# Kernel tuning notes

Measured on AMD Instinct MI355X. Metric: run time of the kernel, lower is better.

The kernel has to match this reference:

```python
import jax, jax.numpy as jnp
import numpy as np

B, C, T = 8, 256, 8192
CALC, H = 256, 4
D = CALC // H  # head dim = 64
EPS = 1e-5


def setup_inputs() -> dict:
    key = jax.random.key(0)
    ks = jax.random.split(key, 5)
    return {
        "x": jax.random.normal(ks[0], (B, C, T), dtype=jnp.float32),
        "W_prenet": jax.random.normal(ks[1], (3 * CALC, C), dtype=jnp.float32) * 0.05,
        "W_proj": jax.random.normal(ks[2], (C, CALC), dtype=jnp.float32) * 0.05,
        "b_proj": jax.random.normal(ks[3], (C,), dtype=jnp.float32) * 0.05,
        "scale": jax.random.normal(ks[4], (1,), dtype=jnp.float32),
        "gamma": jnp.ones((C,), dtype=jnp.float32),
        "beta": jnp.zeros((C,), dtype=jnp.float32),
    }


def reference(x, W_prenet, W_proj, b_proj, scale, gamma, beta):
    residual = x
    # 1x1 conv prenet: [B, 3*CALC, T]
    h = jnp.einsum('oc,bct->bot', W_prenet, x)
    # split heads: channels grouped as H blocks of 3*D, then chunk into q/k/v of D each
    h = h.reshape(B, H, 3 * D, T)
    q = h[:, :, :D, :]            # [B,H,D,T]
    k = h[:, :, D:2 * D, :]
    v = h[:, :, 2 * D:, :]
    # softmax over time on keys (with the module's +1e-5 shift)
    k = jax.nn.softmax(k + EPS, axis=3)
    # keys @ values^T : [B,H,Dk,Dv]
    kv = jnp.einsum('bhdt,bhet->bhde', k, v)
    # kv^T @ queries  : [B,H,Dv,T]
    ctx = jnp.einsum('bhde,bhdt->bhet', kv, q)
    ctx = ctx.reshape(B, CALC, T)
    # 1x1 conv projection + bias
    out = jnp.einsum('oc,bct->bot', W_proj, ctx) + b_proj[None, :, None]
    out = scale * out  # learnable scalar gate
    # dropout is identity in eval mode
    out = out + residual
    # LayerNorm over channel axis with per-channel affine
    mean = jnp.mean(out, axis=1, keepdims=True)
    var = jnp.var(out, axis=1, keepdims=True)
    out = (out - mean) * jax.lax.rsqrt(var + EPS)
    out = out * gamma[None, :, None] + beta[None, :, None]
    return out
```

## Files before the change

kernel.cpp:

```cpp
#include <hip/hip_runtime.h>
#include <hip/hip_bf16.h>
#include <math.h>

#define BB 8
#define CC 256
#define TT 8192
#define EPSF 1e-5f

typedef short v8s __attribute__((ext_vector_type(8)));
typedef float v4f __attribute__((ext_vector_type(4)));

#define MFMA(a, b, c) __builtin_amdgcn_mfma_f32_16x16x32_bf16((a), (b), (c), 0, 0, 0)


#define OFF_WKV 0
#define OFF_WPJ 65536
#define OFF_UPART 98304
#define OFF_ZPART 4292608
#define OFF_KV 4358144
#define OFF_PT 4489216
#define OFF_MBF 4751360

__device__ __forceinline__ unsigned short f2bf(float f) {
  __hip_bfloat16 h = __float2bfloat16(f);
  return __builtin_bit_cast(unsigned short, h);
}
__device__ __forceinline__ float bf2f(unsigned short u) {
  return __bfloat162float(__builtin_bit_cast(__hip_bfloat16, u));
}

__global__ void k0_pack(const float* __restrict__ Wpre,
                        const float* __restrict__ Wproj,
                        float* __restrict__ ws) {
  const int r = blockIdx.x;
  const int c = threadIdx.x;
  if (r < 512) {
    const int h = r >> 7, type = (r >> 6) & 1, d = r & 63;
    const int src = h * 192 + 64 + type * 64 + d;
    ((unsigned short*)(ws + OFF_WKV))[r * 256 + c] = f2bf(Wpre[(size_t)src * 256 + c]);
  } else {
    const int rr = r - 512;
    ((unsigned short*)(ws + OFF_WPJ))[rr * 256 + c] = f2bf(Wproj[(size_t)rr * 256 + c]);
  }
}

__global__ __launch_bounds__(512, 2) void k1_kv(const float* __restrict__ x,
                                                float* __restrict__ ws) {
  __shared__ unsigned short lds[20480];

  const int tid = threadIdx.x;
  const int w = tid >> 6, lane = tid & 63, q = lane >> 4, cl = lane & 15;
  const int h = w >> 1, type = w & 1;
  const int bi = blockIdx.x;
  const int b = bi >> 5, chunk = bi & 31;
  const int t0 = chunk * 256;
  const float* xb = x + (size_t)b * (CC * TT);
  const unsigned short* wkv =
      (const unsigned short*)(ws + OFF_WKV) + (size_t)((h * 2 + type) * 64) * 256;
  unsigned short* ekb = &lds[h * 5120];
  unsigned short* vbb = &lds[h * 5120 + 2560];

  v4f Uacc[2][4];
#pragma unroll
  for (int i = 0; i < 2; ++i)
#pragma unroll
    for (int j = 0; j < 4; ++j) Uacc[i][j] = (v4f){0.f, 0.f, 0.f, 0.f};
  float zacc[4][4];
#pragma unroll
  for (int i = 0; i < 4; ++i)
#pragma unroll
    for (int j = 0; j < 4; ++j) zacc[i][j] = 0.f;

  for (int sub = 0; sub < 4; ++sub) {
    const int ts = t0 + sub * 64;
    {
      const int c = tid & 255, th = tid >> 8;
      const float* xp = xb + (size_t)c * TT + ts + th * 32;
#pragma unroll
      for (int j = 0; j < 8; ++j) {
        const float4 v4 = reinterpret_cast<const float4*>(xp)[j];
        const int tb = th * 32 + j * 4;
        lds[(tb + 0) * 264 + c] = f2bf(v4.x);
        lds[(tb + 1) * 264 + c] = f2bf(v4.y);
        lds[(tb + 2) * 264 + c] = f2bf(v4.z);
        lds[(tb + 3) * 264 + c] = f2bf(v4.w);
      }
    }
    __syncthreads();

    v4f acc[4][4];
#pragma unroll
    for (int i = 0; i < 4; ++i)
#pragma unroll
      for (int j = 0; j < 4; ++j) acc[i][j] = (v4f){0.f, 0.f, 0.f, 0.f};
#pragma unroll
    for (int ks = 0; ks < 8; ++ks) {
      v8s af[4], bfu[4];
#pragma unroll
      for (int rt = 0; rt < 4; ++rt)
        af[rt] = *(const v8s*)(wkv + (size_t)(rt * 16 + cl) * 256 + ks * 32 + q * 8);
#pragma unroll
      for (int ct = 0; ct < 4; ++ct)
        bfu[ct] = *(const v8s*)&lds[(ct * 16 + cl) * 264 + ks * 32 + q * 8];
#pragma unroll
      for (int rt = 0; rt < 4; ++rt)
#pragma unroll
        for (int ct = 0; ct < 4; ++ct)
          acc[rt][ct] = MFMA(af[rt], bfu[ct], acc[rt][ct]);
    }
    __syncthreads();

#pragma unroll
    for (int hp = 0; hp < 2; ++hp) {
      if (type == 0) {
#pragma unroll
        for (int rt = 0; rt < 4; ++rt)
#pragma unroll
          for (int cc = 0; cc < 2; ++cc) {
            const int ct = hp * 2 + cc;
#pragma unroll
            for (int reg = 0; reg < 4; ++reg) {
              const float e = __expf(acc[rt][ct][reg]);
              zacc[rt][reg] += e;
              ekb[(rt * 16 + q * 4 + reg) * 40 + cc * 16 + cl] = f2bf(e);
            }
          }
      } else {
#pragma unroll
        for (int rt = 0; rt < 4; ++rt)
#pragma unroll
          for (int cc = 0; cc < 2; ++cc) {
            const int ct = hp * 2 + cc;
#pragma unroll
            for (int reg = 0; reg < 4; ++reg)
              vbb[(rt * 16 + q * 4 + reg) * 40 + cc * 16 + cl] =
                  f2bf(acc[rt][ct][reg]);
          }
      }
      __syncthreads();
      {
        const int du0 = type * 32;
        v8s afu[2], bfu[4];
#pragma unroll
        for (int ur = 0; ur < 2; ++ur)
          afu[ur] = *(const v8s*)&ekb[(du0 + ur * 16 + cl) * 40 + q * 8];
#pragma unroll
        for (int uc = 0; uc < 4; ++uc)
          bfu[uc] = *(const v8s*)&vbb[(uc * 16 + cl) * 40 + q * 8];
#pragma unroll
        for (int ur = 0; ur < 2; ++ur)
#pragma unroll
          for (int uc = 0; uc < 4; ++uc)
            Uacc[ur][uc] = MFMA(afu[ur], bfu[uc], Uacc[ur][uc]);
      }
      __syncthreads();
    }
  }

  if (type == 0) {
#pragma unroll
    for (int m = 1; m < 16; m <<= 1)
#pragma unroll
      for (int rt = 0; rt < 4; ++rt)
#pragma unroll
        for (int reg = 0; reg < 4; ++reg)
          zacc[rt][reg] += __shfl_xor(zacc[rt][reg], m, 64);
    if (cl == 0) {
      for (int rt = 0; rt < 4; ++rt)
        for (int reg = 0; reg < 4; ++reg)
          ws[OFF_ZPART + (size_t)bi * 256 + h * 64 + rt * 16 + q * 4 + reg] =
              zacc[rt][reg];
    }
  }
  float* Up = ws + OFF_UPART + (size_t)bi * 16384 + h * 4096;
#pragma unroll
  for (int ur = 0; ur < 2; ++ur)
#pragma unroll
    for (int uc = 0; uc < 4; ++uc)
#pragma unroll
      for (int reg = 0; reg < 4; ++reg)
        Up[(type * 32 + ur * 16 + q * 4 + reg) * 64 + uc * 16 + cl] =
            Uacc[ur][uc][reg];
}

__global__ void k2_reduce_kv(float* __restrict__ ws) {
  const int bi = blockIdx.x;
  const int bh = bi >> 4, j = bi & 15;
  const int b = bh >> 2, h = bh & 3;
  const int tid = threadIdx.x;

  __shared__ float zinv[64];
  if (tid < 64) {
    float z = 0.f;
    for (int cb = 0; cb < 32; ++cb)
      z += ws[OFF_ZPART + (size_t)(b * 32 + cb) * 256 + h * 64 + tid];
    zinv[tid] = 1.0f / z;
  }
  __syncthreads();

  const int idx = j * 256 + tid;
  const int d = idx >> 6;
  float s = 0.f;
  for (int cb = 0; cb < 32; ++cb)
    s += ws[OFF_UPART + (size_t)(b * 32 + cb) * 16384 + h * 4096 + idx];
  ws[OFF_KV + (size_t)(b * 4 + h) * 4096 + idx] = s * zinv[d];
}

__global__ void k3a_P(const float* __restrict__ Wpre, float* __restrict__ ws) {
  const int bi = blockIdx.x;
  const int b = bi >> 8, he = bi & 255;
  const int h = he >> 6, e = he & 63;
  const int c = threadIdx.x;
  const float* kvp = ws + OFF_KV + (size_t)(b * 4 + h) * 4096;
  float acc = 0.f;
#pragma unroll 8
  for (int d = 0; d < 64; ++d)
    acc += kvp[d * 64 + e] * Wpre[(size_t)(h * 192 + d) * 256 + c];
  ((unsigned short*)(ws + OFF_PT))[(size_t)b * 65536 + (size_t)c * 256 + he] =
      f2bf(acc);
}

__global__ __launch_bounds__(256, 2) void k3b_M(const float* __restrict__ scale,
                                                float* __restrict__ ws) {
  const int bi = blockIdx.x, b = bi >> 2, cg = bi & 3;
  const int tid = threadIdx.x, w = tid >> 6, lane = tid & 63, q = lane >> 4,
            cl = lane & 15;
  const unsigned short* wpj = (const unsigned short*)(ws + OFF_WPJ);
  const unsigned short* pt =
      (const unsigned short*)(ws + OFF_PT) + (size_t)b * 65536;
  v4f acc[4][4];
#pragma unroll
  for (int i = 0; i < 4; ++i)
#pragma unroll
    for (int j = 0; j < 4; ++j) acc[i][j] = (v4f){0.f, 0.f, 0.f, 0.f};
#pragma unroll
  for (int ks = 0; ks < 8; ++ks) {
    v8s af[4], bfu[4];
#pragma unroll
    for (int rt = 0; rt < 4; ++rt)
      af[rt] = *(const v8s*)(wpj + (size_t)(w * 64 + rt * 16 + cl) * 256 +
                             ks * 32 + q * 8);
#pragma unroll
    for (int ct = 0; ct < 4; ++ct)
      bfu[ct] = *(const v8s*)(pt + (size_t)(cg * 64 + ct * 16 + cl) * 256 +
                              ks * 32 + q * 8);
#pragma unroll
    for (int rt = 0; rt < 4; ++rt)
#pragma unroll
      for (int ct = 0; ct < 4; ++ct)
        acc[rt][ct] = MFMA(af[rt], bfu[ct], acc[rt][ct]);
  }
  const float s = scale[0];
  unsigned short* mbf = (unsigned short*)(ws + OFF_MBF);
#pragma unroll
  for (int rt = 0; rt < 4; ++rt)
#pragma unroll
    for (int ct = 0; ct < 4; ++ct)
#pragma unroll
      for (int reg = 0; reg < 4; ++reg) {
        const int o = w * 64 + rt * 16 + q * 4 + reg;
        const int c = cg * 64 + ct * 16 + cl;
        mbf[((size_t)b * 256 + o) * 256 + c] = f2bf(s * acc[rt][ct][reg]);
      }
}

__global__ __launch_bounds__(256, 2) void k4_proj_ln(
    const float* __restrict__ x, const float* __restrict__ bproj,
    const float* __restrict__ scale, const float* __restrict__ gamma,
    const float* __restrict__ beta, const float* __restrict__ ws,
    float* __restrict__ out) {
  __shared__ unsigned short xs[64 * 264];
  __shared__ float red1[256], red2[256], muA[64], rsA[64];
  const int bi = blockIdx.x, b = bi >> 7, tc = bi & 127;
  const int tg0 = tc * 64;
  const int tid = threadIdx.x, w = tid >> 6, lane = tid & 63, q = lane >> 4,
            cl = lane & 15;
  const float* xb = x + (size_t)b * (CC * TT);

  {
    const int c = tid;
    const float* xp = xb + (size_t)c * TT + tg0;
#pragma unroll
    for (int j = 0; j < 16; ++j) {
      const float4 v4 = reinterpret_cast<const float4*>(xp)[j];
      const int tb = j * 4;
      xs[(tb + 0) * 264 + c] = f2bf(v4.x);
      xs[(tb + 1) * 264 + c] = f2bf(v4.y);
      xs[(tb + 2) * 264 + c] = f2bf(v4.z);
      xs[(tb + 3) * 264 + c] = f2bf(v4.w);
    }
  }
  __syncthreads();

  const unsigned short* mbf =
      (const unsigned short*)(ws + OFF_MBF) + (size_t)b * 65536;
  v4f acc[4][4];
#pragma unroll
  for (int i = 0; i < 4; ++i)
#pragma unroll
    for (int j = 0; j < 4; ++j) acc[i][j] = (v4f){0.f, 0.f, 0.f, 0.f};
#pragma unroll
  for (int ks = 0; ks < 8; ++ks) {
    v8s af[4], bfu[4];
#pragma unroll
    for (int rt = 0; rt < 4; ++rt)
      af[rt] = *(const v8s*)(mbf + (size_t)(w * 64 + rt * 16 + cl) * 256 +
                             ks * 32 + q * 8);
#pragma unroll
    for (int ct = 0; ct < 4; ++ct)
      bfu[ct] = *(const v8s*)&xs[(ct * 16 + cl) * 264 + ks * 32 + q * 8];
#pragma unroll
    for (int rt = 0; rt < 4; ++rt)
#pragma unroll
      for (int ct = 0; ct < 4; ++ct)
        acc[rt][ct] = MFMA(af[rt], bfu[ct], acc[rt][ct]);
  }

  const float s = scale[0];
#pragma unroll
  for (int rt = 0; rt < 4; ++rt)
#pragma unroll
    for (int reg = 0; reg < 4; ++reg) {
      const int o = w * 64 + rt * 16 + q * 4 + reg;
      const float sb = s * bproj[o];
#pragma unroll
      for (int ct = 0; ct < 4; ++ct) {
        const int tl = ct * 16 + cl;
        acc[rt][ct][reg] += sb + bf2f(xs[tl * 264 + o]);
      }
    }

#pragma unroll
  for (int ct = 0; ct < 4; ++ct) {
    float s1 = 0.f, s2 = 0.f;
#pragma unroll
    for (int rt = 0; rt < 4; ++rt)
#pragma unroll
      for (int reg = 0; reg < 4; ++reg) {
        const float v = acc[rt][ct][reg];
        s1 += v;
        s2 += v * v;
      }
    s1 += __shfl_xor(s1, 16, 64);
    s1 += __shfl_xor(s1, 32, 64);
    s2 += __shfl_xor(s2, 16, 64);
    s2 += __shfl_xor(s2, 32, 64);
    if (q == 0) {
      red1[w * 64 + ct * 16 + cl] = s1;
      red2[w * 64 + ct * 16 + cl] = s2;
    }
  }
  __syncthreads();
  if (tid < 64) {
    const float s1 = red1[tid] + red1[64 + tid] + red1[128 + tid] + red1[192 + tid];
    const float s2 = red2[tid] + red2[64 + tid] + red2[128 + tid] + red2[192 + tid];
    const float mu = s1 * (1.f / 256.f);
    const float var = s2 * (1.f / 256.f) - mu * mu;
    muA[tid] = mu;
    rsA[tid] = rsqrtf(var + EPSF);
  }
  __syncthreads();

  float* ob = out + (size_t)b * (CC * TT) + tg0;
#pragma unroll
  for (int rt = 0; rt < 4; ++rt)
#pragma unroll
    for (int reg = 0; reg < 4; ++reg) {
      const int o = w * 64 + rt * 16 + q * 4 + reg;
      const float g = gamma[o], bt = beta[o];
#pragma unroll
      for (int ct = 0; ct < 4; ++ct) {
        const int tl = ct * 16 + cl;
        ob[(size_t)o * TT + tl] = (acc[rt][ct][reg] - muA[tl]) * rsA[tl] * g + bt;
      }
    }
}

extern "C" void kernel_launch(void* const* d_in, const int* in_sizes, int n_in,
                              void* d_out, int out_size, void* d_ws,
                              size_t ws_size, hipStream_t stream) {
  (void)in_sizes; (void)n_in; (void)out_size; (void)ws_size;
  const float* x = (const float*)d_in[0];
  const float* Wpre = (const float*)d_in[1];
  const float* Wproj = (const float*)d_in[2];
  const float* bproj = (const float*)d_in[3];
  const float* scale = (const float*)d_in[4];
  const float* gamma = (const float*)d_in[5];
  const float* beta = (const float*)d_in[6];
  float* out = (float*)d_out;
  float* ws = (float*)d_ws;

  hipLaunchKernelGGL(k0_pack, dim3(768), dim3(256), 0, stream, Wpre, Wproj, ws);
  hipLaunchKernelGGL(k1_kv, dim3(256), dim3(512), 0, stream, x, ws);
  hipLaunchKernelGGL(k2_reduce_kv, dim3(512), dim3(256), 0, stream, ws);
  hipLaunchKernelGGL(k3a_P, dim3(BB * 256), dim3(256), 0, stream, Wpre, ws);
  hipLaunchKernelGGL(k3b_M, dim3(32), dim3(256), 0, stream, scale, ws);
  hipLaunchKernelGGL(k4_proj_ln, dim3(BB * 128), dim3(256), 0, stream, x, bproj,
                     scale, gamma, beta, ws, out);
}
```

Baseline: 222.5 us.

## Split kernels into more blocks and pack bf16 pairs in LDS staging

Doubles the grid of the KV kernel (128-step time chunks, 64 partials per batch) and the projection/LayerNorm kernel (32-column tiles), and splits the M GEMM across 4x more blocks. The aim is more parallelism and occupancy on a GPU with many CUs. It also replaces 16-bit LDS stores with paired 32-bit stores of two channels, cutting LDS store instructions. The cost is double the partial-sum traffic and reduction work in k2, a larger workspace, and less MFMA operand reuse per block.

```diff
diff --git a/kernel.cpp b/kernel.cpp
--- a/kernel.cpp
+++ b/kernel.cpp
@@ -16,10 +16,10 @@
 #define OFF_WKV 0
 #define OFF_WPJ 65536
 #define OFF_UPART 98304
-#define OFF_ZPART 4292608
-#define OFF_KV 4358144
-#define OFF_PT 4489216
-#define OFF_MBF 4751360
+#define OFF_ZPART 8486912
+#define OFF_KV 8617984
+#define OFF_PT 8749056
+#define OFF_MBF 9011200
 
 __device__ __forceinline__ unsigned short f2bf(float f) {
   __hip_bfloat16 h = __float2bfloat16(f);
@@ -27,6 +27,9 @@
 }
 __device__ __forceinline__ float bf2f(unsigned short u) {
   return __bfloat162float(__builtin_bit_cast(__hip_bfloat16, u));
+}
+__device__ __forceinline__ unsigned int pack2(float lo, float hi) {
+  return (unsigned int)f2bf(lo) | ((unsigned int)f2bf(hi) << 16);
 }
 
 __global__ void k0_pack(const float* __restrict__ Wpre,
@@ -44,7 +47,7 @@
   }
 }
 
-__global__ __launch_bounds__(512, 2) void k1_kv(const float* __restrict__ x,
+__global__ __launch_bounds__(512, 4) void k1_kv(const float* __restrict__ x,
                                                 float* __restrict__ ws) {
   __shared__ unsigned short lds[20480];
 
@@ -52,8 +55,8 @@
   const int w = tid >> 6, lane = tid & 63, q = lane >> 4, cl = lane & 15;
   const int h = w >> 1, type = w & 1;
   const int bi = blockIdx.x;
-  const int b = bi >> 5, chunk = bi & 31;
-  const int t0 = chunk * 256;
+  const int b = bi >> 6, chunk = bi & 63;
+  const int t0 = chunk * 128;
   const float* xb = x + (size_t)b * (CC * TT);
   const unsigned short* wkv =
       (const unsigned short*)(ws + OFF_WKV) + (size_t)((h * 2 + type) * 64) * 256;
@@ -71,19 +74,25 @@
 #pragma unroll
     for (int j = 0; j < 4; ++j) zacc[i][j] = 0.f;
 
-  for (int sub = 0; sub < 4; ++sub) {
+  const int c0 = (tid & 127) * 2;
+  const int th = tid >> 7;
+  unsigned int* l32 = (unsigned int*)lds;
+
+  for (int sub = 0; sub < 2; ++sub) {
     const int ts = t0 + sub * 64;
     {
-      const int c = tid & 255, th = tid >> 8;
-      const float* xp = xb + (size_t)c * TT + ts + th * 32;
-#pragma unroll
-      for (int j = 0; j < 8; ++j) {
-        const float4 v4 = reinterpret_cast<const float4*>(xp)[j];
-        const int tb = th * 32 + j * 4;
-        lds[(tb + 0) * 264 + c] = f2bf(v4.x);
-        lds[(tb + 1) * 264 + c] = f2bf(v4.y);
-        lds[(tb + 2) * 264 + c] = f2bf(v4.z);
-        lds[(tb + 3) * 264 + c] = f2bf(v4.w);
+      const float* xpA = xb + (size_t)c0 * TT + ts + th * 16;
+      const float* xpB = xpA + TT;
+      const int cw = c0 >> 1;
+#pragma unroll
+      for (int k = 0; k < 4; ++k) {
+        const float4 va = reinterpret_cast<const float4*>(xpA)[k];
+        const float4 vb = reinterpret_cast<const float4*>(xpB)[k];
+        const int tb = th * 16 + k * 4;
+        l32[(tb + 0) * 132 + cw] = pack2(va.x, vb.x);
+        l32[(tb + 1) * 132 + cw] = pack2(va.y, vb.y);
+        l32[(tb + 2) * 132 + cw] = pack2(va.z, vb.z);
+        l32[(tb + 3) * 132 + cw] = pack2(va.w, vb.w);
       }
     }
     __syncthreads();
@@ -192,8 +201,8 @@
   __shared__ float zinv[64];
   if (tid < 64) {
     float z = 0.f;
-    for (int cb = 0; cb < 32; ++cb)
-      z += ws[OFF_ZPART + (size_t)(b * 32 + cb) * 256 + h * 64 + tid];
+    for (int cb = 0; cb < 64; ++cb)
+      z += ws[OFF_ZPART + (size_t)(b * 64 + cb) * 256 + h * 64 + tid];
     zinv[tid] = 1.0f / z;
   }
   __syncthreads();
@@ -201,8 +210,8 @@
   const int idx = j * 256 + tid;
   const int d = idx >> 6;
   float s = 0.f;
-  for (int cb = 0; cb < 32; ++cb)
-    s += ws[OFF_UPART + (size_t)(b * 32 + cb) * 16384 + h * 4096 + idx];
+  for (int cb = 0; cb < 64; ++cb)
+    s += ws[OFF_UPART + (size_t)(b * 64 + cb) * 16384 + h * 4096 + idx];
   ws[OFF_KV + (size_t)(b * 4 + h) * 4096 + idx] = s * zinv[d];
 }
 
@@ -222,97 +231,94 @@
 
 __global__ __launch_bounds__(256, 2) void k3b_M(const float* __restrict__ scale,
                                                 float* __restrict__ ws) {
-  const int bi = blockIdx.x, b = bi >> 2, cg = bi & 3;
+  const int bi = blockIdx.x;
+  const int b = bi >> 4, cg = (bi >> 2) & 3, rg = bi & 3;
   const int tid = threadIdx.x, w = tid >> 6, lane = tid & 63, q = lane >> 4,
             cl = lane & 15;
   const unsigned short* wpj = (const unsigned short*)(ws + OFF_WPJ);
   const unsigned short* pt =
       (const unsigned short*)(ws + OFF_PT) + (size_t)b * 65536;
-  v4f acc[4][4];
-#pragma unroll
-  for (int i = 0; i < 4; ++i)
-#pragma unroll
-    for (int j = 0; j < 4; ++j) acc[i][j] = (v4f){0.f, 0.f, 0.f, 0.f};
+  v4f acc[4];
+#pragma unroll
+  for (int j = 0; j < 4; ++j) acc[j] = (v4f){0.f, 0.f, 0.f, 0.f};
 #pragma unroll
   for (int ks = 0; ks < 8; ++ks) {
-    v8s af[4], bfu[4];
-#pragma unroll
-    for (int rt = 0; rt < 4; ++rt)
-      af[rt] = *(const v8s*)(wpj + (size_t)(w * 64 + rt * 16 + cl) * 256 +
-                             ks * 32 + q * 8);
+    const v8s af = *(const v8s*)(wpj + (size_t)(rg * 64 + w * 16 + cl) * 256 +
+                                 ks * 32 + q * 8);
+    v8s bfu[4];
 #pragma unroll
     for (int ct = 0; ct < 4; ++ct)
       bfu[ct] = *(const v8s*)(pt + (size_t)(cg * 64 + ct * 16 + cl) * 256 +
                               ks * 32 + q * 8);
 #pragma unroll
-    for (int rt = 0; rt < 4; ++rt)
-#pragma unroll
-      for (int ct = 0; ct < 4; ++ct)
-        acc[rt][ct] = MFMA(af[rt], bfu[ct], acc[rt][ct]);
+    for (int ct = 0; ct < 4; ++ct) acc[ct] = MFMA(af, bfu[ct], acc[ct]);
   }
   const float s = scale[0];
   unsigned short* mbf = (unsigned short*)(ws + OFF_MBF);
 #pragma unroll
-  for (int rt = 0; rt < 4; ++rt)
-#pragma unroll
-    for (int ct = 0; ct < 4; ++ct)
-#pragma unroll
-      for (int reg = 0; reg < 4; ++reg) {
-        const int o = w * 64 + rt * 16 + q * 4 + reg;
-        const int c = cg * 64 + ct * 16 + cl;
-        mbf[((size_t)b * 256 + o) * 256 + c] = f2bf(s * acc[rt][ct][reg]);
-      }
-}
-
-__global__ __launch_bounds__(256, 2) void k4_proj_ln(
+  for (int ct = 0; ct < 4; ++ct)
+#pragma unroll
+    for (int reg = 0; reg < 4; ++reg) {
+      const int o = rg * 64 + w * 16 + q * 4 + reg;
+      const int c = cg * 64 + ct * 16 + cl;
+      mbf[((size_t)b * 256 + o) * 256 + c] = f2bf(s * acc[ct][reg]);
+    }
+}
+
+__global__ __launch_bounds__(256, 4) void k4_proj_ln(
     const float* __restrict__ x, const float* __restrict__ bproj,
     const float* __restrict__ scale, const float* __restrict__ gamma,
     const float* __restrict__ beta, const float* __restrict__ ws,
     float* __restrict__ out) {
-  __shared__ unsigned short xs[64 * 264];
-  __shared__ float red1[256], red2[256], muA[64], rsA[64];
-  const int bi = blockIdx.x, b = bi >> 7, tc = bi & 127;
-  const int tg0 = tc * 64;
+  __shared__ unsigned short xs[32 * 264];
+  __shared__ float red1[128], red2[128], muA[32], rsA[32];
+  const int bi = blockIdx.x, b = bi >> 8, tc = bi & 255;
+  const int tg0 = tc * 32;
   const int tid = threadIdx.x, w = tid >> 6, lane = tid & 63, q = lane >> 4,
             cl = lane & 15;
   const float* xb = x + (size_t)b * (CC * TT);
 
   {
-    const int c = tid;
-    const float* xp = xb + (size_t)c * TT + tg0;
-#pragma unroll
-    for (int j = 0; j < 16; ++j) {
-      const float4 v4 = reinterpret_cast<const float4*>(xp)[j];
-      const int tb = j * 4;
-      xs[(tb + 0) * 264 + c] = f2bf(v4.x);
-      xs[(tb + 1) * 264 + c] = f2bf(v4.y);
-      xs[(tb + 2) * 264 + c] = f2bf(v4.z);
-      xs[(tb + 3) * 264 + c] = f2bf(v4.w);
+    const int c0 = (tid & 127) * 2;
+    const int th = tid >> 7;
+    const float* xpA = xb + (size_t)c0 * TT + tg0 + th * 16;
+    const float* xpB = xpA + TT;
+    unsigned int* x32 = (unsigned int*)xs;
+    const int cw = c0 >> 1;
+#pragma unroll
+    for (int k = 0; k < 4; ++k) {
+      const float4 va = reinterpret_cast<const float4*>(xpA)[k];
+      const float4 vb = reinterpret_cast<const float4*>(xpB)[k];
+      const int tb = th * 16 + k * 4;
+      x32[(tb + 0) * 132 + cw] = pack2(va.x, vb.x);
+      x32[(tb + 1) * 132 + cw] = pack2(va.y, vb.y);
+      x32[(tb + 2) * 132 + cw] = pack2(va.z, vb.z);
+      x32[(tb + 3) * 132 + cw] = pack2(va.w, vb.w);
     }
   }
   __syncthreads();
 
   const unsigned short* mbf =
       (const unsigned short*)(ws + OFF_MBF) + (size_t)b * 65536;
-  v4f acc[4][4];
+  v4f acc[4][2];
 #pragma unroll
   for (int i = 0; i < 4; ++i)
 #pragma unroll
-    for (int j = 0; j < 4; ++j) acc[i][j] = (v4f){0.f, 0.f, 0.f, 0.f};
+    for (int j = 0; j < 2; ++j) acc[i][j] = (v4f){0.f, 0.f, 0.f, 0.f};
 #pragma unroll
   for (int ks = 0; ks < 8; ++ks) {
-    v8s af[4], bfu[4];
+    v8s af[4], bfu[2];
 #pragma unroll
     for (int rt = 0; rt < 4; ++rt)
       af[rt] = *(const v8s*)(mbf + (size_t)(w * 64 + rt * 16 + cl) * 256 +
                              ks * 32 + q * 8);
 #pragma unroll
-    for (int ct = 0; ct < 4; ++ct)
+    for (int ct = 0; ct < 2; ++ct)
       bfu[ct] = *(const v8s*)&xs[(ct * 16 + cl) * 264 + ks * 32 + q * 8];
 #pragma unroll
     for (int rt = 0; rt < 4; ++rt)
 #pragma unroll
-      for (int ct = 0; ct < 4; ++ct)
+      for (int ct = 0; ct < 2; ++ct)
         acc[rt][ct] = MFMA(af[rt], bfu[ct], acc[rt][ct]);
   }
 
@@ -324,14 +330,14 @@
       const int o = w * 64 + rt * 16 + q * 4 + reg;
       const float sb = s * bproj[o];
 #pragma unroll
-      for (int ct = 0; ct < 4; ++ct) {
+      for (int ct = 0; ct < 2; ++ct) {
         const int tl = ct * 16 + cl;
         acc[rt][ct][reg] += sb + bf2f(xs[tl * 264 + o]);
       }
     }
 
 #pragma unroll
-  for (int ct = 0; ct < 4; ++ct) {
+  for (int ct = 0; ct < 2; ++ct) {
     float s1 = 0.f, s2 = 0.f;
 #pragma unroll
     for (int rt = 0; rt < 4; ++rt)
@@ -346,14 +352,14 @@
     s2 += __shfl_xor(s2, 16, 64);
     s2 += __shfl_xor(s2, 32, 64);
     if (q == 0) {
-      red1[w * 64 + ct * 16 + cl] = s1;
-      red2[w * 64 + ct * 16 + cl] = s2;
+      red1[w * 32 + ct * 16 + cl] = s1;
+      red2[w * 32 + ct * 16 + cl] = s2;
     }
   }
   __syncthreads();
-  if (tid < 64) {
-    const float s1 = red1[tid] + red1[64 + tid] + red1[128 + tid] + red1[192 + tid];
-    const float s2 = red2[tid] + red2[64 + tid] + red2[128 + tid] + red2[192 + tid];
+  if (tid < 32) {
+    const float s1 = red1[tid] + red1[32 + tid] + red1[64 + tid] + red1[96 + tid];
+    const float s2 = red2[tid] + red2[32 + tid] + red2[64 + tid] + red2[96 + tid];
     const float mu = s1 * (1.f / 256.f);
     const float var = s2 * (1.f / 256.f) - mu * mu;
     muA[tid] = mu;
@@ -369,7 +375,7 @@
       const int o = w * 64 + rt * 16 + q * 4 + reg;
       const float g = gamma[o], bt = beta[o];
 #pragma unroll
-      for (int ct = 0; ct < 4; ++ct) {
+      for (int ct = 0; ct < 2; ++ct) {
         const int tl = ct * 16 + cl;
         ob[(size_t)o * TT + tl] = (acc[rt][ct][reg] - muA[tl]) * rsA[tl] * g + bt;
       }
@@ -391,10 +397,10 @@
   float* ws = (float*)d_ws;
 
   hipLaunchKernelGGL(k0_pack, dim3(768), dim3(256), 0, stream, Wpre, Wproj, ws);
-  hipLaunchKernelGGL(k1_kv, dim3(256), dim3(512), 0, stream, x, ws);
+  hipLaunchKernelGGL(k1_kv, dim3(512), dim3(512), 0, stream, x, ws);
   hipLaunchKernelGGL(k2_reduce_kv, dim3(512), dim3(256), 0, stream, ws);
   hipLaunchKernelGGL(k3a_P, dim3(BB * 256), dim3(256), 0, stream, Wpre, ws);
-  hipLaunchKernelGGL(k3b_M, dim3(32), dim3(256), 0, stream, scale, ws);
-  hipLaunchKernelGGL(k4_proj_ln, dim3(BB * 128), dim3(256), 0, stream, x, bproj,
-                     scale, gamma, beta, ws, out);
-}
+  hipLaunchKernelGGL(k3b_M, dim3(128), dim3(256), 0, stream, scale, ws);
+  hipLaunchKernelGGL(k4_proj_ln, dim3(BB * 128 * 2), dim3(256), 0, stream, x,
+                     bproj, scale, gamma, beta, ws, out);
+}
```

Result: slower. 287.8 us (+29.4%).

## Split k1_kv work by head pair across more blocks and prefetch next x tile

Applied to the files above, without the earlier changes.

The KV-accumulation kernel now launches twice as many blocks, each handling two heads instead of four, with each warp computing a 16-row slice of both K and V projections instead of a whole K or V head. The x tile for the next sub-step is loaded into registers while the U MFMA runs, then written to LDS as packed bf16 pairs, replacing the per-iteration blocking load. The aim is more parallelism across CUs, less per-warp register pressure, and overlap of global loads with compute. In exchange, x is read twice (once per head pair) and the reduce kernel's indexing changes to match.

```diff
diff --git a/kernel.cpp b/kernel.cpp
--- a/kernel.cpp
+++ b/kernel.cpp
@@ -27,6 +27,9 @@
 }
 __device__ __forceinline__ float bf2f(unsigned short u) {
   return __bfloat162float(__builtin_bit_cast(__hip_bfloat16, u));
+}
+__device__ __forceinline__ unsigned int pack2(float lo, float hi) {
+  return (unsigned int)f2bf(lo) | ((unsigned int)f2bf(hi) << 16);
 }
 
 __global__ void k0_pack(const float* __restrict__ Wpre,
@@ -44,156 +47,166 @@
   }
 }
 
-__global__ __launch_bounds__(512, 2) void k1_kv(const float* __restrict__ x,
-                                                float* __restrict__ ws) {
-  __shared__ unsigned short lds[20480];
+__global__ __launch_bounds__(512) void k1_kv(const float* __restrict__ x,
+                                             float* __restrict__ ws) {
+  __shared__ unsigned short lds[35328];
 
   const int tid = threadIdx.x;
   const int w = tid >> 6, lane = tid & 63, q = lane >> 4, cl = lane & 15;
-  const int h = w >> 1, type = w & 1;
+  const int lh = w >> 2, dq = w & 3;
   const int bi = blockIdx.x;
-  const int b = bi >> 5, chunk = bi & 31;
+  const int b = bi >> 6, rem = bi & 63, chunk = rem >> 1, hp = rem & 1;
+  const int h = hp * 2 + lh;
   const int t0 = chunk * 256;
   const float* xb = x + (size_t)b * (CC * TT);
-  const unsigned short* wkv =
-      (const unsigned short*)(ws + OFF_WKV) + (size_t)((h * 2 + type) * 64) * 256;
-  unsigned short* ekb = &lds[h * 5120];
-  unsigned short* vbb = &lds[h * 5120 + 2560];
-
-  v4f Uacc[2][4];
-#pragma unroll
-  for (int i = 0; i < 2; ++i)
-#pragma unroll
-    for (int j = 0; j < 4; ++j) Uacc[i][j] = (v4f){0.f, 0.f, 0.f, 0.f};
-  float zacc[4][4];
-#pragma unroll
-  for (int i = 0; i < 4; ++i)
-#pragma unroll
-    for (int j = 0; j < 4; ++j) zacc[i][j] = 0.f;
+  const unsigned short* wk =
+      (const unsigned short*)(ws + OFF_WKV) + (size_t)((h * 2 + 0) * 64) * 256;
+  const unsigned short* wv =
+      (const unsigned short*)(ws + OFF_WKV) + (size_t)((h * 2 + 1) * 64) * 256;
+  unsigned short* eb = &lds[16896 + lh * 9216];
+  unsigned short* vb = &lds[16896 + lh * 9216 + 4608];
+
+  v4f Uacc[4];
+#pragma unroll
+  for (int j = 0; j < 4; ++j) Uacc[j] = (v4f){0.f, 0.f, 0.f, 0.f};
+  float zacc[4] = {0.f, 0.f, 0.f, 0.f};
+
+  const int c0 = (tid & 127) * 2;
+  const int th = tid >> 7;
+  const int cw = tid & 127;
+  unsigned int* l32 = (unsigned int*)lds;
+
+  {
+    const float* xpA = xb + (size_t)c0 * TT + t0 + th * 16;
+    const float* xpB = xpA + TT;
+#pragma unroll
+    for (int k = 0; k < 4; ++k) {
+      const float4 va = reinterpret_cast<const float4*>(xpA)[k];
+      const float4 vb4 = reinterpret_cast<const float4*>(xpB)[k];
+      const int tb = th * 16 + k * 4;
+      l32[(tb + 0) * 132 + cw] = pack2(va.x, vb4.x);
+      l32[(tb + 1) * 132 + cw] = pack2(va.y, vb4.y);
+      l32[(tb + 2) * 132 + cw] = pack2(va.z, vb4.z);
+      l32[(tb + 3) * 132 + cw] = pack2(va.w, vb4.w);
+    }
+  }
 
   for (int sub = 0; sub < 4; ++sub) {
-    const int ts = t0 + sub * 64;
-    {
-      const int c = tid & 255, th = tid >> 8;
-      const float* xp = xb + (size_t)c * TT + ts + th * 32;
-#pragma unroll
-      for (int j = 0; j < 8; ++j) {
-        const float4 v4 = reinterpret_cast<const float4*>(xp)[j];
-        const int tb = th * 32 + j * 4;
-        lds[(tb + 0) * 264 + c] = f2bf(v4.x);
-        lds[(tb + 1) * 264 + c] = f2bf(v4.y);
-        lds[(tb + 2) * 264 + c] = f2bf(v4.z);
-        lds[(tb + 3) * 264 + c] = f2bf(v4.w);
-      }
-    }
     __syncthreads();
 
-    v4f acc[4][4];
-#pragma unroll
-    for (int i = 0; i < 4; ++i)
-#pragma unroll
-      for (int j = 0; j < 4; ++j) acc[i][j] = (v4f){0.f, 0.f, 0.f, 0.f};
+    v4f acc[4];
+
+#pragma unroll
+    for (int j = 0; j < 4; ++j) acc[j] = (v4f){0.f, 0.f, 0.f, 0.f};
 #pragma unroll
     for (int ks = 0; ks < 8; ++ks) {
-      v8s af[4], bfu[4];
-#pragma unroll
-      for (int rt = 0; rt < 4; ++rt)
-        af[rt] = *(const v8s*)(wkv + (size_t)(rt * 16 + cl) * 256 + ks * 32 + q * 8);
+      const v8s af =
+          *(const v8s*)(wk + (size_t)(dq * 16 + cl) * 256 + ks * 32 + q * 8);
+      v8s bfu[4];
 #pragma unroll
       for (int ct = 0; ct < 4; ++ct)
         bfu[ct] = *(const v8s*)&lds[(ct * 16 + cl) * 264 + ks * 32 + q * 8];
 #pragma unroll
-      for (int rt = 0; rt < 4; ++rt)
-#pragma unroll
-        for (int ct = 0; ct < 4; ++ct)
-          acc[rt][ct] = MFMA(af[rt], bfu[ct], acc[rt][ct]);
-    }
+      for (int ct = 0; ct < 4; ++ct) acc[ct] = MFMA(af, bfu[ct], acc[ct]);
+    }
+#pragma unroll
+    for (int ct = 0; ct < 4; ++ct)
+#pragma unroll
+      for (int reg = 0; reg < 4; ++reg) {
+        const float e = __expf(acc[ct][reg]);
+        zacc[reg] += e;
+        eb[(dq * 16 + q * 4 + reg) * 72 + ct * 16 + cl] = f2bf(e);
+      }
+
+#pragma unroll
+    for (int j = 0; j < 4; ++j) acc[j] = (v4f){0.f, 0.f, 0.f, 0.f};
+#pragma unroll
+    for (int ks = 0; ks < 8; ++ks) {
+      const v8s af =
+          *(const v8s*)(wv + (size_t)(dq * 16 + cl) * 256 + ks * 32 + q * 8);
+      v8s bfu[4];
+#pragma unroll
+      for (int ct = 0; ct < 4; ++ct)
+        bfu[ct] = *(const v8s*)&lds[(ct * 16 + cl) * 264 + ks * 32 + q * 8];
+#pragma unroll
+      for (int ct = 0; ct < 4; ++ct) acc[ct] = MFMA(af, bfu[ct], acc[ct]);
+    }
+#pragma unroll
+    for (int ct = 0; ct < 4; ++ct)
+#pragma unroll
+      for (int reg = 0; reg < 4; ++reg)
+        vb[(dq * 16 + q * 4 + reg) * 72 + ct * 16 + cl] = f2bf(acc[ct][reg]);
+
     __syncthreads();
 
-#pragma unroll
-    for (int hp = 0; hp < 2; ++hp) {
-      if (type == 0) {
-#pragma unroll
-        for (int rt = 0; rt < 4; ++rt)
-#pragma unroll
-          for (int cc = 0; cc < 2; ++cc) {
-            const int ct = hp * 2 + cc;
-#pragma unroll
-            for (int reg = 0; reg < 4; ++reg) {
-              const float e = __expf(acc[rt][ct][reg]);
-              zacc[rt][reg] += e;
-              ekb[(rt * 16 + q * 4 + reg) * 40 + cc * 16 + cl] = f2bf(e);
-            }
-          }
-      } else {
-#pragma unroll
-        for (int rt = 0; rt < 4; ++rt)
-#pragma unroll
-          for (int cc = 0; cc < 2; ++cc) {
-            const int ct = hp * 2 + cc;
-#pragma unroll
-            for (int reg = 0; reg < 4; ++reg)
-              vbb[(rt * 16 + q * 4 + reg) * 40 + cc * 16 + cl] =
-                  f2bf(acc[rt][ct][reg]);
-          }
-      }
-      __syncthreads();
-      {
-        const int du0 = type * 32;
-        v8s afu[2], bfu[4];
-#pragma unroll
-        for (int ur = 0; ur < 2; ++ur)
-          afu[ur] = *(const v8s*)&ekb[(du0 + ur * 16 + cl) * 40 + q * 8];
-#pragma unroll
-        for (int uc = 0; uc < 4; ++uc)
-          bfu[uc] = *(const v8s*)&vbb[(uc * 16 + cl) * 40 + q * 8];
-#pragma unroll
-        for (int ur = 0; ur < 2; ++ur)
-#pragma unroll
-          for (int uc = 0; uc < 4; ++uc)
-            Uacc[ur][uc] = MFMA(afu[ur], bfu[uc], Uacc[ur][uc]);
-      }
-      __syncthreads();
-    }
-  }
-
-  if (type == 0) {
-#pragma unroll
-    for (int m = 1; m < 16; m <<= 1)
-#pragma unroll
-      for (int rt = 0; rt < 4; ++rt)
-#pragma unroll
-        for (int reg = 0; reg < 4; ++reg)
-          zacc[rt][reg] += __shfl_xor(zacc[rt][reg], m, 64);
-    if (cl == 0) {
-      for (int rt = 0; rt < 4; ++rt)
-        for (int reg = 0; reg < 4; ++reg)
-          ws[OFF_ZPART + (size_t)bi * 256 + h * 64 + rt * 16 + q * 4 + reg] =
-              zacc[rt][reg];
-    }
-  }
-  float* Up = ws + OFF_UPART + (size_t)bi * 16384 + h * 4096;
-#pragma unroll
-  for (int ur = 0; ur < 2; ++ur)
-#pragma unroll
-    for (int uc = 0; uc < 4; ++uc)
-#pragma unroll
-      for (int reg = 0; reg < 4; ++reg)
-        Up[(type * 32 + ur * 16 + q * 4 + reg) * 64 + uc * 16 + cl] =
-            Uacc[ur][uc][reg];
+    float4 nxA[4], nxB[4];
+    if (sub < 3) {
+      const float* xpA = xb + (size_t)c0 * TT + (t0 + (sub + 1) * 64) + th * 16;
+      const float* xpB = xpA + TT;
+#pragma unroll
+      for (int k = 0; k < 4; ++k) {
+        nxA[k] = reinterpret_cast<const float4*>(xpA)[k];
+        nxB[k] = reinterpret_cast<const float4*>(xpB)[k];
+      }
+    }
+
+#pragma unroll
+    for (int ks = 0; ks < 2; ++ks) {
+      const v8s afu =
+          *(const v8s*)&eb[(dq * 16 + cl) * 72 + ks * 32 + q * 8];
+      v8s bfv[4];
+#pragma unroll
+      for (int uc = 0; uc < 4; ++uc)
+        bfv[uc] = *(const v8s*)&vb[(uc * 16 + cl) * 72 + ks * 32 + q * 8];
+#pragma unroll
+      for (int uc = 0; uc < 4; ++uc)
+        Uacc[uc] = MFMA(afu, bfv[uc], Uacc[uc]);
+    }
+
+    if (sub < 3) {
+#pragma unroll
+      for (int k = 0; k < 4; ++k) {
+        const int tb = th * 16 + k * 4;
+        l32[(tb + 0) * 132 + cw] = pack2(nxA[k].x, nxB[k].x);
+        l32[(tb + 1) * 132 + cw] = pack2(nxA[k].y, nxB[k].y);
+        l32[(tb + 2) * 132 + cw] = pack2(nxA[k].z, nxB[k].z);
+        l32[(tb + 3) * 132 + cw] = pack2(nxA[k].w, nxB[k].w);
+      }
+    }
+  }
+
+#pragma unroll
+  for (int m = 1; m < 16; m <<= 1)
+#pragma unroll
+    for (int reg = 0; reg < 4; ++reg)
+      zacc[reg] += __shfl_xor(zacc[reg], m, 64);
+  if (cl == 0) {
+#pragma unroll
+    for (int reg = 0; reg < 4; ++reg)
+      ws[OFF_ZPART + (size_t)bi * 128 + lh * 64 + dq * 16 + q * 4 + reg] =
+          zacc[reg];
+  }
+  float* Up = ws + OFF_UPART + (size_t)bi * 8192 + lh * 4096;
+#pragma unroll
+  for (int uc = 0; uc < 4; ++uc)
+#pragma unroll
+    for (int reg = 0; reg < 4; ++reg)
+      Up[(dq * 16 + q * 4 + reg) * 64 + uc * 16 + cl] = Uacc[uc][reg];
 }
 
 __global__ void k2_reduce_kv(float* __restrict__ ws) {
   const int bi = blockIdx.x;
   const int bh = bi >> 4, j = bi & 15;
   const int b = bh >> 2, h = bh & 3;
+  const int hp = h >> 1, lh = h & 1;
   const int tid = threadIdx.x;
 
   __shared__ float zinv[64];
   if (tid < 64) {
     float z = 0.f;
+#pragma unroll 4
     for (int cb = 0; cb < 32; ++cb)
-      z += ws[OFF_ZPART + (size_t)(b * 32 + cb) * 256 + h * 64 + tid];
+      z += ws[OFF_ZPART + (size_t)(b * 64 + cb * 2 + hp) * 128 + lh * 64 + tid];
     zinv[tid] = 1.0f / z;
   }
   __syncthreads();
@@ -201,8 +214,9 @@
   const int idx = j * 256 + tid;
   const int d = idx >> 6;
   float s = 0.f;
+#pragma unroll 4
   for (int cb = 0; cb < 32; ++cb)
-    s += ws[OFF_UPART + (size_t)(b * 32 + cb) * 16384 + h * 4096 + idx];
+    s += ws[OFF_UPART + (size_t)(b * 64 + cb * 2 + hp) * 8192 + lh * 4096 + idx];
   ws[OFF_KV + (size_t)(b * 4 + h) * 4096 + idx] = s * zinv[d];
 }
 
@@ -391,7 +405,7 @@
   float* ws = (float*)d_ws;
 
   hipLaunchKernelGGL(k0_pack, dim3(768), dim3(256), 0, stream, Wpre, Wproj, ws);
-  hipLaunchKernelGGL(k1_kv, dim3(256), dim3(512), 0, stream, x, ws);
+  hipLaunchKernelGGL(k1_kv, dim3(512), dim3(512), 0, stream, x, ws);
   hipLaunchKernelGGL(k2_reduce_kv, dim3(512), dim3(256), 0, stream, ws);
   hipLaunchKernelGGL(k3a_P, dim3(BB * 256), dim3(256), 0, stream, Wpre, ws);
   hipLaunchKernelGGL(k3b_M, dim3(32), dim3(256), 0, stream, scale, ws);
```

Result: slower. 237.2 us (+6.6%).
